# Performance work log

Measured on AMD Instinct MI355X. Metric: run time of the kernel, lower is better.

## Reference

```python
import jax, jax.numpy as jnp
import numpy as np
import math

NX = 4096   # input features (last_dim)
NY = 4096   # units
REDUCTION = 0.5  # param_reduction


def _make_window(nx, ny, reduction):
    """Faithful vectorized port of SzDense.build for form='diagonal', halfbandwidth=0."""
    hw = nx * ny / math.sqrt(nx * nx + ny * ny) * (1.0 - math.sqrt(reduction))
    rxy = (nx - 1) / (ny - 1)
    hwdiv = hw * math.sqrt(rxy * rxy + 1.0)
    iy = np.arange(ny, dtype=np.float64)
    c1 = rxy * iy - hwdiv
    # int(c1)+1 when c1>=0 (truncation == floor for nonneg), else 0
    ix1 = np.where(c1 >= 0, np.floor(c1).astype(np.int64) + 1, 0)
    c2 = rxy * iy + hwdiv
    ix2 = np.where(c2 < nx, np.ceil(c2).astype(np.int64), nx)
    ix = np.arange(nx)[:, None]
    wnd = ((ix >= ix1[None, :]) & (ix < ix2[None, :])).astype(np.float32)
    num_ones = float(wnd.sum())
    w_corr = (nx * ny) / num_ones if num_ones > 0 else 1.0
    return wnd, np.float32(w_corr)


def setup_inputs() -> dict:
    key = jax.random.key(0)
    kx, kk, kb = jax.random.split(key, 3)
    x = jax.random.normal(kx, (4096, NX), dtype=jnp.float32)
    wnd_np, w_corr = _make_window(NX, NY, REDUCTION)
    window = jnp.asarray(wnd_np)
    # glorot-uniform-like init, then build()'s kernel.assign(kernel * wnd * w_corr)
    limit = math.sqrt(6.0 / (NX + NY))
    kernel = jax.random.uniform(kk, (NX, NY), dtype=jnp.float32, minval=-limit, maxval=limit)
    kernel = kernel * window * w_corr
    bias = jnp.zeros((NY,), dtype=jnp.float32)
    return {"x": x, "kernel": kernel, "window": window, "bias": bias}


def reference(x, kernel, window, bias):
    # SzDense.call: dense(inputs, kernel * window, bias, activation=None)
    return jnp.matmul(x, kernel * window) + bias
```

## Files before the change

### kernel.cpp

```cpp
#include <hip/hip_runtime.h>
#include <hip/hip_bf16.h>
#include <stdint.h>

#define MM 4096
#define NN 4096
#define KK 4096
#define BM 128
#define BN 128
#define BK 64

typedef __bf16 bf16;
typedef __attribute__((ext_vector_type(8))) __bf16 bf16x8;
typedef __attribute__((ext_vector_type(4))) __bf16 bf16x4;
typedef __attribute__((ext_vector_type(4))) float f32x4;

__device__ inline const __attribute__((address_space(1))) void* to_global(const void* p) {
    return (const __attribute__((address_space(1))) void*)p;
}
__device__ inline __attribute__((address_space(3))) void* to_local(void* p) {
    return (__attribute__((address_space(3))) void*)p;
}

#define LDN 68
#define NBX 8192
__global__ void prep(const float* __restrict__ x,
                     const float* __restrict__ w,
                     const float* __restrict__ wnd,
                     bf16* __restrict__ Abf,
                     bf16* __restrict__ bt) {
    __shared__ bf16 Ts[64][LDN];
    const int t = threadIdx.x;
    int b = blockIdx.x;
    if (b < NBX) {
        size_t i = ((size_t)b * 256 + t) * 8;
        float4 v0 = *(const float4*)(x + i);
        float4 v1 = *(const float4*)(x + i + 4);
        bf16x8 o;
        o[0] = (bf16)v0.x; o[1] = (bf16)v0.y; o[2] = (bf16)v0.z; o[3] = (bf16)v0.w;
        o[4] = (bf16)v1.x; o[5] = (bf16)v1.y; o[6] = (bf16)v1.z; o[7] = (bf16)v1.w;
        *(bf16x8*)(Abf + i) = o;
        return;
    }
    b -= NBX;
    const int k0 = (b >> 6) * 64;
    const int n0 = (b & 63) * 64;

    {
        const int nc = (t & 15) * 4;
        const int kb = t >> 4;
        #pragma unroll
        for (int p = 0; p < 4; ++p) {
            const int kl = p * 16 + kb;
            size_t idx = (size_t)(k0 + kl) * NN + (n0 + nc);
            float4 a = *(const float4*)(w + idx);
            float4 m = *(const float4*)(wnd + idx);
            bf16x4 o;
            o[0] = (bf16)(a.x * m.x);
            o[1] = (bf16)(a.y * m.y);
            o[2] = (bf16)(a.z * m.z);
            o[3] = (bf16)(a.w * m.w);
            *(bf16x4*)&Ts[kl][nc] = o;
        }
    }
    __syncthreads();

    {
        const int nl = t >> 2;
        #pragma unroll
        for (int p = 0; p < 2; ++p) {
            const int kc = (t & 3) + 4 * p;
            bf16x8 o;
            #pragma unroll
            for (int i = 0; i < 8; ++i) o[i] = Ts[kc * 8 + i][nl];
            *(bf16x8*)&bt[(size_t)(n0 + nl) * KK + k0 + kc * 8] = o;
        }
    }
}

__global__ __launch_bounds__(256, 4) void gemm_bt_bias(
    const bf16* __restrict__ A,
    const bf16* __restrict__ Bt,
    const float* __restrict__ bias,
    float* __restrict__ C) {
    __shared__ bf16 As[BM * BK];
    __shared__ bf16 Bs[BN * BK];

    const int t = threadIdx.x;
    const int wave = t >> 6;
    const int lane = t & 63;
    const int quad = lane >> 4;
    const int l15 = lane & 15;

    const int flat = blockIdx.y * 32 + blockIdx.x;
    const int xcd = flat & 7;
    const int idx = flat >> 3;
    const int n_tile = xcd * 4 + (idx & 3);
    const int m_tile = idx >> 2;
    const int m0 = m_tile * BM;
    const int n0 = n_tile * BN;

    const int wm = wave >> 1;
    const int wn = wave & 1;

    f32x4 acc[4][4];
    #pragma unroll
    for (int i = 0; i < 4; ++i)
        #pragma unroll
        for (int j = 0; j < 4; ++j)
            acc[i][j] = (f32x4)0.0f;

    const int row_s = t >> 3;
    const int col_s = (((t & 7) ^ ((t >> 3) & 7))) * 8;
    const bf16* Ag = A + (size_t)(m0 + row_s) * KK + col_s;
    const bf16* Bg = Bt + (size_t)(n0 + row_s) * KK + col_s;

    for (int k0 = 0; k0 < KK; k0 += BK) {
        #pragma unroll
        for (int c = 0; c < 4; ++c) {
            __builtin_amdgcn_global_load_lds(
                to_global(Ag + k0 + (size_t)c * 32 * KK),
                to_local(As + ((size_t)c * 256 + wave * 64) * 8), 16, 0, 0);
            __builtin_amdgcn_global_load_lds(
                to_global(Bg + k0 + (size_t)c * 32 * KK),
                to_local(Bs + ((size_t)c * 256 + wave * 64) * 8), 16, 0, 0);
        }
        __syncthreads();

        #pragma unroll
        for (int s = 0; s < 2; ++s) {
            bf16x8 af[4], bfr[4];
            #pragma unroll
            for (int i = 0; i < 4; ++i) {
                const int R = wm * 64 + i * 16 + l15;
                const int g = (s * 4 + quad) ^ (l15 & 7);
                af[i] = *(const bf16x8*)&As[R * BK + g * 8];
            }
            #pragma unroll
            for (int j = 0; j < 4; ++j) {
                const int R = wn * 64 + j * 16 + l15;
                const int g = (s * 4 + quad) ^ (l15 & 7);
                bfr[j] = *(const bf16x8*)&Bs[R * BK + g * 8];
            }
            #pragma unroll
            for (int i = 0; i < 4; ++i)
                #pragma unroll
                for (int j = 0; j < 4; ++j)
                    acc[i][j] = __builtin_amdgcn_mfma_f32_16x16x32_bf16(af[i], bfr[j], acc[i][j], 0, 0, 0);
        }

        __syncthreads();
    }

    #pragma unroll
    for (int i = 0; i < 4; ++i) {
        #pragma unroll
        for (int j = 0; j < 4; ++j) {
            int col = n0 + wn * 64 + j * 16 + l15;
            float b = bias[col];
            #pragma unroll
            for (int r = 0; r < 4; ++r) {
                int row = m0 + wm * 64 + i * 16 + quad * 4 + r;
                C[(size_t)row * NN + col] = acc[i][j][r] + b;
            }
        }
    }
}

extern "C" void kernel_launch(void* const* d_in, const int* in_sizes, int n_in,
                              void* d_out, int out_size, void* d_ws, size_t ws_size,
                              hipStream_t stream) {
    const float* x = (const float*)d_in[0];
    const float* kern = (const float*)d_in[1];
    const float* wnd = (const float*)d_in[2];
    const float* bias = (const float*)d_in[3];
    float* out = (float*)d_out;

    bf16* Abf = (bf16*)d_ws;
    bf16* Btbf = (bf16*)((char*)d_ws + (size_t)MM * KK * sizeof(bf16));

    prep<<<NBX + (NN / 64) * (KK / 64), 256, 0, stream>>>(x, kern, wnd, Abf, Btbf);
    gemm_bt_bias<<<dim3(32, 32), 256, 0, stream>>>(Abf, Btbf, bias, out);
}
```

Baseline: 330.9 us.

## Double-buffer LDS tiles in bf16 GEMM to overlap global loads with MFMA

Splits the A and B shared-memory tiles into two buffers. The next K-slice is issued with global_load_lds into the idle buffer while MFMAs consume the current one, with the main loop unrolled by two K-steps. The aim is to hide global-to-LDS load latency behind compute. LDS use per block doubles to 64KB and launch bounds drop from 4 to 2 blocks per CU, so there are fewer resident waves to hide latency. The compiler's waitcnt handling may also serialise the overlapped loads.

```diff
diff --git a/kernel.cpp b/kernel.cpp
--- a/kernel.cpp
+++ b/kernel.cpp
@@ -77,13 +77,13 @@
     }
 }
 
-__global__ __launch_bounds__(256, 4) void gemm_bt_bias(
+__global__ __launch_bounds__(256, 2) void gemm_bt_bias(
     const bf16* __restrict__ A,
     const bf16* __restrict__ Bt,
     const float* __restrict__ bias,
     float* __restrict__ C) {
-    __shared__ bf16 As[BM * BK];
-    __shared__ bf16 Bs[BN * BK];
+    __shared__ bf16 As[2][BM * BK];
+    __shared__ bf16 Bs[2][BN * BK];
 
     const int t = threadIdx.x;
     const int wave = t >> 6;
@@ -110,46 +110,60 @@
             acc[i][j] = (f32x4)0.0f;
 
     const int row_s = t >> 3;
-    const int col_s = (((t & 7) ^ ((t >> 3) & 7))) * 8;
+    const int col_s = ((t & 7) ^ ((t >> 3) & 7)) * 8;
     const bf16* Ag = A + (size_t)(m0 + row_s) * KK + col_s;
     const bf16* Bg = Bt + (size_t)(n0 + row_s) * KK + col_s;
 
-    for (int k0 = 0; k0 < KK; k0 += BK) {
-        #pragma unroll
-        for (int c = 0; c < 4; ++c) {
-            __builtin_amdgcn_global_load_lds(
-                to_global(Ag + k0 + (size_t)c * 32 * KK),
-                to_local(As + ((size_t)c * 256 + wave * 64) * 8), 16, 0, 0);
-            __builtin_amdgcn_global_load_lds(
-                to_global(Bg + k0 + (size_t)c * 32 * KK),
-                to_local(Bs + ((size_t)c * 256 + wave * 64) * 8), 16, 0, 0);
-        }
+#define ISSUE(K0, P)                                                          \
+    {                                                                         \
+        _Pragma("unroll")                                                     \
+        for (int c = 0; c < 4; ++c) {                                         \
+            __builtin_amdgcn_global_load_lds(                                 \
+                to_global(Ag + (K0) + (size_t)c * 32 * KK),                   \
+                to_local(&As[P][((size_t)c * 256 + wave * 64) * 8]), 16, 0, 0);\
+            __builtin_amdgcn_global_load_lds(                                 \
+                to_global(Bg + (K0) + (size_t)c * 32 * KK),                   \
+                to_local(&Bs[P][((size_t)c * 256 + wave * 64) * 8]), 16, 0, 0);\
+        }                                                                     \
+    }
+
+#define COMPUTE(P)                                                            \
+    {                                                                         \
+        _Pragma("unroll")                                                     \
+        for (int s = 0; s < 2; ++s) {                                         \
+            bf16x8 af[4], bfr[4];                                             \
+            _Pragma("unroll")                                                 \
+            for (int i = 0; i < 4; ++i) {                                     \
+                const int R = wm * 64 + i * 16 + l15;                         \
+                const int g = (s * 4 + quad) ^ (l15 & 7);                     \
+                af[i] = *(const bf16x8*)&As[P][R * BK + g * 8];               \
+            }                                                                 \
+            _Pragma("unroll")                                                 \
+            for (int j = 0; j < 4; ++j) {                                     \
+                const int R = wn * 64 + j * 16 + l15;                         \
+                const int g = (s * 4 + quad) ^ (l15 & 7);                     \
+                bfr[j] = *(const bf16x8*)&Bs[P][R * BK + g * 8];              \
+            }                                                                 \
+            _Pragma("unroll")                                                 \
+            for (int i = 0; i < 4; ++i)                                       \
+                _Pragma("unroll")                                             \
+                for (int j = 0; j < 4; ++j)                                   \
+                    acc[i][j] = __builtin_amdgcn_mfma_f32_16x16x32_bf16(      \
+                        af[i], bfr[j], acc[i][j], 0, 0, 0);                   \
+        }                                                                     \
+    }
+
+    ISSUE(0, 0);
+    for (int k0 = 0; k0 < KK; k0 += 2 * BK) {
         __syncthreads();
-
-        #pragma unroll
-        for (int s = 0; s < 2; ++s) {
-            bf16x8 af[4], bfr[4];
-            #pragma unroll
-            for (int i = 0; i < 4; ++i) {
-                const int R = wm * 64 + i * 16 + l15;
-                const int g = (s * 4 + quad) ^ (l15 & 7);
-                af[i] = *(const bf16x8*)&As[R * BK + g * 8];
-            }
-            #pragma unroll
-            for (int j = 0; j < 4; ++j) {
-                const int R = wn * 64 + j * 16 + l15;
-                const int g = (s * 4 + quad) ^ (l15 & 7);
-                bfr[j] = *(const bf16x8*)&Bs[R * BK + g * 8];
-            }
-            #pragma unroll
-            for (int i = 0; i < 4; ++i)
-                #pragma unroll
-                for (int j = 0; j < 4; ++j)
-                    acc[i][j] = __builtin_amdgcn_mfma_f32_16x16x32_bf16(af[i], bfr[j], acc[i][j], 0, 0, 0);
-        }
-
+        ISSUE(k0 + BK, 1);
+        COMPUTE(0);
         __syncthreads();
+        if (k0 + 2 * BK < KK) ISSUE(k0 + 2 * BK, 0);
+        COMPUTE(1);
     }
+#undef ISSUE
+#undef COMPUTE
 
     #pragma unroll
     for (int i = 0; i < 4; ++i) {
```

After: 364.2 us. 1.1x slower.
